# Performance work log

Hardware: AMD Instinct MI355X
Metric: run time of the kernel (lower is better)

Reference implementation:

```python
import jax, jax.numpy as jnp
import numpy as np

N_FOOD = 50000
N_NUT = 50000
E = 800000
D = 128      # embedding_dim == hidden_dim
H = 4        # heads
C = D // H   # per-head channels
L = 2        # num_layers
NEG_SLOPE = 0.2


def _gat_conv(x_src, x_dst, ei, Wsrc, Wdst, a_src, a_dst, bias, n_dst):
    """PyG GATConv (bipartite, no self loops, concat heads, no edge_dim)."""
    hs = (x_src @ Wsrc).reshape(-1, H, C)   # [Ns, H, C]
    hd = (x_dst @ Wdst).reshape(-1, H, C)   # [Nd, H, C]
    src, dst = ei[0], ei[1]
    alpha_s = jnp.einsum('nhc,hc->nh', hs, a_src)  # [Ns, H]
    alpha_d = jnp.einsum('nhc,hc->nh', hd, a_dst)  # [Nd, H]
    e = alpha_s[src] + alpha_d[dst]                # [E, H]
    e = jax.nn.leaky_relu(e, NEG_SLOPE)
    # segment softmax over edges grouped by destination node
    emax = jax.ops.segment_max(e, dst, num_segments=n_dst)
    emax = jnp.where(jnp.isfinite(emax), emax, 0.0)
    ex = jnp.exp(e - emax[dst])
    denom = jax.ops.segment_sum(ex, dst, num_segments=n_dst)
    alpha = ex / (denom[dst] + 1e-16)              # [E, H]
    msg = hs[src] * alpha[:, :, None]              # [E, H, C]
    out = jax.ops.segment_sum(msg, dst, num_segments=n_dst)
    return out.reshape(n_dst, H * C) + bias


def setup_inputs() -> dict:
    key = jax.random.key(0)
    ks = jax.random.split(key, 16)
    w = 1.0 / np.sqrt(D)
    a = 1.0 / np.sqrt(C)
    inp = {
        'x_food': jax.random.normal(ks[0], (N_FOOD, D), jnp.float32),
        'x_nut': jax.random.normal(ks[1], (N_NUT, D), jnp.float32),
        'Wsrc_fn': jax.random.normal(ks[2], (L, D, D), jnp.float32) * w,
        'Wdst_fn': jax.random.normal(ks[3], (L, D, D), jnp.float32) * w,
        'att_src_fn': jax.random.normal(ks[4], (L, H, C), jnp.float32) * a,
        'att_dst_fn': jax.random.normal(ks[5], (L, H, C), jnp.float32) * a,
        'bias_fn': jnp.zeros((L, D), jnp.float32),
        'Wsrc_nf': jax.random.normal(ks[6], (L, D, D), jnp.float32) * w,
        'Wdst_nf': jax.random.normal(ks[7], (L, D, D), jnp.float32) * w,
        'att_src_nf': jax.random.normal(ks[8], (L, H, C), jnp.float32) * a,
        'att_dst_nf': jax.random.normal(ks[9], (L, H, C), jnp.float32) * a,
        'bias_nf': jnp.zeros((L, D), jnp.float32),
        'ei_fn': jax.random.randint(ks[10], (2, E), 0, N_FOOD, jnp.int32),  # food -> nutrient
        'ei_nf': jax.random.randint(ks[11], (2, E), 0, N_NUT, jnp.int32),   # nutrient -> food
    }
    return inp


def reference(x_food, x_nut, Wsrc_fn, Wdst_fn, att_src_fn, att_dst_fn, bias_fn,
              Wsrc_nf, Wdst_nf, att_src_nf, att_dst_nf, bias_nf, ei_fn, ei_nf):
    h_food, h_nut = x_food, x_nut
    for l in range(L):
        # relation food --contains--> nutrient (dst = nutrient)
        out_nut = _gat_conv(h_food, h_nut, ei_fn, Wsrc_fn[l], Wdst_fn[l],
                            att_src_fn[l], att_dst_fn[l], bias_fn[l], N_NUT)
        # relation nutrient --contained_in--> food (dst = food)
        out_food = _gat_conv(h_nut, h_food, ei_nf, Wsrc_nf[l], Wdst_nf[l],
                             att_src_nf[l], att_dst_nf[l], bias_nf[l], N_FOOD)
        # dropout is identity at inference; ELU activation
        h_food = jax.nn.elu(out_food)
        h_nut = jax.nn.elu(out_nut)
    return jnp.stack([h_food, h_nut])  # [2, 50000, 128]
```

## Files before the change

### kernel.cpp

```cpp
#include <hip/hip_runtime.h>
#include <math.h>

#define NNODE 50000
#define NEDGE 800000
#define DIM   128
#define NHEAD 4
#define NTILE ((NNODE + 63) / 64)
#define NBUCK 196
#define ECHUNK 196
#define CAP   6144
#define LOG2E 1.44269504088896340736f

typedef __bf16 bf16x8 __attribute__((ext_vector_type(8)));
typedef float  f32x4  __attribute__((ext_vector_type(4)));
typedef float  f32x2  __attribute__((ext_vector_type(2)));

static __device__ __forceinline__ void bfsplit(float x, ushort& hi, ushort& lo) {
    __bf16 h = (__bf16)x;
    float hf = (float)h;
    __bf16 l = (__bf16)(x - hf);
    hi = __builtin_bit_cast(unsigned short, h);
    lo = __builtin_bit_cast(unsigned short, l);
}
static __device__ __forceinline__ ushort f2h(float x) {
    _Float16 h = (_Float16)x;
    return __builtin_bit_cast(unsigned short, h);
}
static __device__ __forceinline__ f32x2 up2v(unsigned u) {
    f32x2 r;
    r.x = (float)__builtin_bit_cast(_Float16, (unsigned short)(u & 0xffff));
    r.y = (float)__builtin_bit_cast(_Float16, (unsigned short)(u >> 16));
    return r;
}
static __device__ __forceinline__ unsigned encf(float f) {
    unsigned u = __builtin_bit_cast(unsigned, f);
    return (u >> 31) ? ~u : (u | 0x80000000u);
}
static __device__ __forceinline__ float decf(unsigned x) {
    unsigned u = (x >> 31) ? (x & 0x7fffffffu) : ~x;
    return __builtin_bit_cast(float, u);
}

__global__ __launch_bounds__(256) void bhist(const int* __restrict__ eA,
                                             const int* __restrict__ eB,
                                             int* __restrict__ bcnt) {
    int rel = (int)(blockIdx.x >= ECHUNK);
    const int* dstrow = (rel ? eB : eA) + NEDGE;
    int blk = blockIdx.x - rel * ECHUNK;
    __shared__ int hist[256];
    hist[threadIdx.x] = 0;
    __syncthreads();
    int base = blk * 4096;
    #pragma unroll
    for (int k = 0; k < 16; k++) {
        int e = base + k * 256 + threadIdx.x;
        if (e < NEDGE) atomicAdd(&hist[dstrow[e] >> 8], 1);
    }
    __syncthreads();
    int h = hist[threadIdx.x];
    if (h) atomicAdd(&bcnt[rel * 256 + threadIdx.x], h);
}

__global__ __launch_bounds__(256) void bscan(const int* __restrict__ bcnt,
                                             int* __restrict__ bko, int* __restrict__ bcur,
                                             int* __restrict__ ptrA, int* __restrict__ ptrB) {
    int rel = blockIdx.x;
    __shared__ int tmp[256];
    int t = threadIdx.x;
    int v = bcnt[rel * 256 + t];
    tmp[t] = v; __syncthreads();
    for (int off = 1; off < 256; off <<= 1) {
        int a = (t >= off) ? tmp[t - off] : 0; __syncthreads();
        tmp[t] += a; __syncthreads();
    }
    int excl = tmp[t] - v;
    bko[rel * 256 + t] = excl;
    bcur[rel * 256 + t] = excl;
    if (t == 255) (rel ? ptrB : ptrA)[NNODE] = tmp[255];
}

__global__ __launch_bounds__(256) void bscatter(const int* __restrict__ eA,
                                                const int* __restrict__ eB,
                                                int* __restrict__ bcur,
                                                unsigned* __restrict__ bktA,
                                                unsigned* __restrict__ bktB) {
    int rel = (int)(blockIdx.x >= ECHUNK);
    const int* ebase = rel ? eB : eA;
    unsigned* bkt = rel ? bktB : bktA;
    int blk = blockIdx.x - rel * ECHUNK;
    __shared__ int hist[256], bas[256], cur[256];
    hist[threadIdx.x] = 0;
    __syncthreads();
    int base = blk * 4096;
    #pragma unroll
    for (int k = 0; k < 16; k++) {
        int e = base + k * 256 + threadIdx.x;
        if (e < NEDGE) atomicAdd(&hist[ebase[NEDGE + e] >> 8], 1);
    }
    __syncthreads();
    int h = hist[threadIdx.x];
    bas[threadIdx.x] = h ? atomicAdd(&bcur[rel * 256 + threadIdx.x], h) : 0;
    cur[threadIdx.x] = 0;
    __syncthreads();
    #pragma unroll
    for (int k = 0; k < 16; k++) {
        int e = base + k * 256 + threadIdx.x;
        if (e < NEDGE) {
            int s = ebase[e], d = ebase[NEDGE + e];
            int b = d >> 8;
            int loc = atomicAdd(&cur[b], 1);
            bkt[bas[b] + loc] = ((unsigned)(d & 255) << 16) | (unsigned)s;
        }
    }
}

__global__ __launch_bounds__(256) void bsort(const unsigned* __restrict__ bktA,
                                             const unsigned* __restrict__ bktB,
                                             const int* __restrict__ bko,
                                             int* __restrict__ ptrA, int* __restrict__ ptrB,
                                             ushort* __restrict__ srcA, ushort* __restrict__ srcB) {
    int rel = (int)(blockIdx.x >= NBUCK);
    const unsigned* bkt = rel ? bktB : bktA;
    int* ptr   = rel ? ptrB : ptrA;
    ushort* srcs = rel ? srcB : srcA;
    int b = blockIdx.x - rel * NBUCK;
    int beg = bko[rel * 256 + b], end = bko[rel * 256 + b + 1];
    int cnt_e = end - beg;
    __shared__ int hist[256], excl[256], cur[256];
    __shared__ unsigned sorted[CAP];
    int t = threadIdx.x;
    hist[t] = 0;
    __syncthreads();
    for (int i = t; i < cnt_e; i += 256) atomicAdd(&hist[bkt[beg + i] >> 16], 1);
    __syncthreads();
    int v = hist[t];
    excl[t] = v; __syncthreads();
    for (int off = 1; off < 256; off <<= 1) {
        int a = (t >= off) ? excl[t - off] : 0; __syncthreads();
        excl[t] += a; __syncthreads();
    }
    int ex = excl[t] - v;
    int d = b * 256 + t;
    if (d < NNODE) ptr[d] = beg + ex;
    cur[t] = ex;
    __syncthreads();
    for (int i = t; i < cnt_e; i += 256) {
        unsigned u = bkt[beg + i];
        int dl = u >> 16;
        int p = atomicAdd(&cur[dl], 1);
        if (p < CAP) sorted[p] = u;
        else srcs[beg + p] = (ushort)(u & 0xffffu);
    }
    __syncthreads();
    int lim = cnt_e < CAP ? cnt_e : CAP;
    for (int i = t; i < lim; i += 256) {
        unsigned u = sorted[i];
        srcs[beg + i] = (ushort)(u & 0xffffu);
    }
}

__global__ void prep_wav(const float* __restrict__ Wsrc_fn, const float* __restrict__ a_src_fn,
                         const float* __restrict__ Wdst_fn, const float* __restrict__ a_dst_fn,
                         const float* __restrict__ Wsrc_nf, const float* __restrict__ a_src_nf,
                         const float* __restrict__ Wdst_nf, const float* __restrict__ a_dst_nf,
                         float* __restrict__ wav) {
    int call = blockIdx.x;
    int layer = call >> 1, which = call & 1;
    const float* Ws = which ? Wsrc_nf : Wsrc_fn;
    const float* as = which ? a_src_nf : a_src_fn;
    const float* Wd = which ? Wdst_fn : Wdst_nf;
    const float* ad = which ? a_dst_fn : a_dst_nf;
    Ws += layer * DIM * DIM; Wd += layer * DIM * DIM;
    as += layer * DIM; ad += layer * DIM;
    for (int it = threadIdx.x; it < 512; it += 256) {
        int k = it >> 2, h = it & 3;
        float s = 0.f, dv = 0.f;
        #pragma unroll 8
        for (int c = 0; c < 32; c++) {
            s  += Ws[k * DIM + h * 32 + c] * as[h * 32 + c];
            dv += Wd[k * DIM + h * 32 + c] * ad[h * 32 + c];
        }
        float* o = wav + (size_t)call * DIM * 8 + k * 8;
        o[h] = s; o[h + 4] = dv;
    }
}

__global__ __launch_bounds__(256, 3) void transform_kernel(
    const float* __restrict__ XA, const float* __restrict__ WA, const float* __restrict__ wavA,
    ushort* __restrict__ HSA, float* __restrict__ ASA, float* __restrict__ ADA,
    const float* __restrict__ XB, const float* __restrict__ WB, const float* __restrict__ wavB,
    ushort* __restrict__ HSB, float* __restrict__ ASB, float* __restrict__ ADB,
    unsigned* __restrict__ Mg, int nb)
{
    int rel = (int)(blockIdx.x >= (unsigned)nb);
    const float* X  = rel ? XB : XA;
    const float* W  = rel ? WB : WA;
    const float* wav = rel ? wavB : wavA;
    ushort* HS = rel ? HSB : HSA;
    float*  AS = rel ? ASB : ASA;
    float*  AD = rel ? ADB : ADA;

    __shared__ ushort WTh[64][136], WTl[64][136];
    __shared__ ushort wavTh[16][136], wavTl[16][136];
    __shared__ unsigned mloc[4];

    int vb = blockIdx.x - rel * nb;
    int half = vb & 1;
    int ch = half * 64;

    for (int i = threadIdx.x; i < 64 * DIM; i += 256) {
        int col = i & 63, k = i >> 6;
        ushort hi, lo; bfsplit(W[k * DIM + ch + col], hi, lo);
        WTh[col][k] = hi; WTl[col][k] = lo;
    }
    for (int i = threadIdx.x; i < 16 * DIM; i += 256) {
        int c = i & 15, k = i >> 4;
        float w = (c < 8) ? wav[k * 8 + c] : 0.f;
        ushort hi, lo; bfsplit(w, hi, lo);
        wavTh[c][k] = hi; wavTl[c][k] = lo;
    }
    if (threadIdx.x < 4) mloc[threadIdx.x] = 0;
    __syncthreads();

    const int wv = threadIdx.x >> 6, lane = threadIdx.x & 63;
    const int lm = lane & 15, lq = lane >> 4;
    const int r0 = wv * 16;

    for (int tile = vb >> 1; tile < NTILE; tile += (nb >> 1)) {
        int row0 = tile * 64;
        int myrow = row0 + r0 + lm;
        int rowc = myrow < NNODE ? myrow : NNODE - 1;
        const float4* Xr = (const float4*)(X + (size_t)rowc * DIM);

        float4 xv[8];
        #pragma unroll
        for (int kc = 0; kc < 4; kc++) {
            xv[kc * 2]     = Xr[kc * 8 + lq * 2];
            xv[kc * 2 + 1] = Xr[kc * 8 + lq * 2 + 1];
        }

        f32x4 acc[4] = {{0,0,0,0},{0,0,0,0},{0,0,0,0},{0,0,0,0}};
        f32x4 accv = {0,0,0,0};
        #pragma unroll
        for (int kc = 0; kc < 4; kc++) {
            const float* fp = (const float*)&xv[kc * 2];
            bf16x8 ah, al;
            #pragma unroll
            for (int j = 0; j < 8; j++) {
                float x = fp[j];
                __bf16 h = (__bf16)x;
                ah[j] = h;
                al[j] = (__bf16)(x - (float)h);
            }
            int k0 = kc * 32 + lq * 8;
            #pragma unroll
            for (int ct = 0; ct < 4; ct++) {
                bf16x8 bh = *(const bf16x8*)&WTh[ct * 16 + lm][k0];
                bf16x8 bl = *(const bf16x8*)&WTl[ct * 16 + lm][k0];
                acc[ct] = __builtin_amdgcn_mfma_f32_16x16x32_bf16(al, bh, acc[ct], 0, 0, 0);
                acc[ct] = __builtin_amdgcn_mfma_f32_16x16x32_bf16(ah, bl, acc[ct], 0, 0, 0);
                acc[ct] = __builtin_amdgcn_mfma_f32_16x16x32_bf16(ah, bh, acc[ct], 0, 0, 0);
            }
            if (half == 0) {
                bf16x8 vh = *(const bf16x8*)&wavTh[lm][k0];
                bf16x8 vl = *(const bf16x8*)&wavTl[lm][k0];
                accv = __builtin_amdgcn_mfma_f32_16x16x32_bf16(al, vh, accv, 0, 0, 0);
                accv = __builtin_amdgcn_mfma_f32_16x16x32_bf16(ah, vl, accv, 0, 0, 0);
                accv = __builtin_amdgcn_mfma_f32_16x16x32_bf16(ah, vh, accv, 0, 0, 0);
            }
        }

        #pragma unroll
        for (int ct = 0; ct < 4; ct++) {
            #pragma unroll
            for (int r = 0; r < 4; r++) {
                int row = row0 + r0 + lq * 4 + r;
                if (row < NNODE) HS[(size_t)row * DIM + ch + ct * 16 + lm] = f2h(acc[ct][r]);
            }
        }
        if (half == 0 && lm < 8) {
            accv *= LOG2E;
            float mx4 = -INFINITY;
            #pragma unroll
            for (int r = 0; r < 4; r++) {
                int row = row0 + r0 + lq * 4 + r;
                if (row < NNODE) {
                    if (lm < 4) AS[row * 4 + lm] = accv[r];
                    else        AD[row * 4 + (lm - 4)] = accv[r];
                }
                mx4 = fmaxf(mx4, accv[r]);
            }
            if (lm < 4) atomicMax(&mloc[lm], encf(mx4));
        }
    }
    __syncthreads();
    if (half == 0 && threadIdx.x < 4)
        atomicMax(&Mg[rel * 4 + threadIdx.x], mloc[threadIdx.x]);
}

__global__ __launch_bounds__(256) void agg_kernel(
    const ushort* __restrict__ HSA, const float* __restrict__ ASA, const float* __restrict__ ADA,
    const int* __restrict__ ptrA, const ushort* __restrict__ srcA,
    const float* __restrict__ biasA, float* __restrict__ outA,
    const ushort* __restrict__ HSB, const float* __restrict__ ASB, const float* __restrict__ ADB,
    const int* __restrict__ ptrB, const ushort* __restrict__ srcB,
    const float* __restrict__ biasB, float* __restrict__ outB,
    const unsigned* __restrict__ Mg, int nb)
{
    int rel = (int)(blockIdx.x >= (unsigned)nb);
    const uint4* HS4 = (const uint4*)(rel ? HSB : HSA);
    const float* AS = rel ? ASB : ASA;
    const float* AD = rel ? ADB : ADA;
    const ushort* srcs = rel ? srcB : srcA;
    const int* ptr = rel ? ptrB : ptrA;
    const float* bias = rel ? biasB : biasA;
    float* out = rel ? outB : outA;

    int bid = blockIdx.x - rel * nb;
    int wave = threadIdx.x >> 6, lane = threadIdx.x & 63;
    int d = bid * 4 + wave;
    if (d >= NNODE) return;

    int q  = lane >> 4;
    int li = lane & 15;
    int hh = li >> 2;

    float ad_h = AD[d * 4 + hh];
    float mm = decf(Mg[rel * 4 + hh]) + ad_h;
    mm = mm > 0.f ? mm : 0.2f * mm;

    int e0 = ptr[d], e1 = ptr[d + 1];

    float acc[8] = {0.f,0.f,0.f,0.f,0.f,0.f,0.f,0.f};
    float l = 0.f;

    int e = e0;
    for (; e + 8 <= e1; e += 8) {
        int iA = e + q, iB = e + 4 + q;
        int sA = srcs[iA], sB = srcs[iB];
        uint4 hA = HS4[sA * 16 + li];
        uint4 hB = HS4[sB * 16 + li];
        float aA = AS[sA * 4 + hh];
        float aB = AS[sB * 4 + hh];
        float vA = aA + ad_h; vA = fmaxf(vA, 0.2f * vA);
        float vB = aB + ad_h; vB = fmaxf(vB, 0.2f * vB);
        float pA = __builtin_amdgcn_exp2f(vA - mm);
        float pB = __builtin_amdgcn_exp2f(vB - mm);
        l += pA + pB;
        #pragma unroll
        for (int j = 0; j < 4; j++) {
            f32x2 h2A = up2v(((const unsigned*)&hA)[j]);
            f32x2 h2B = up2v(((const unsigned*)&hB)[j]);
            acc[2*j]   += h2A.x * pA + h2B.x * pB;
            acc[2*j+1] += h2A.y * pA + h2B.y * pB;
        }
    }
    for (; e < e1; e += 4) {
        int ee = e + q;
        bool act = ee < e1;
        int eidx = act ? ee : e1 - 1;
        int s = srcs[eidx];
        uint4 hv = HS4[s * 16 + li];
        float av = AS[s * 4 + hh];
        float v = av + ad_h; v = fmaxf(v, 0.2f * v);
        float p = __builtin_amdgcn_exp2f(v - mm);
        p = act ? p : 0.f;
        l += p;
        #pragma unroll
        for (int j = 0; j < 4; j++) {
            f32x2 h2 = up2v(((const unsigned*)&hv)[j]);
            acc[2*j]   += h2.x * p;
            acc[2*j+1] += h2.y * p;
        }
    }

    #pragma unroll
    for (int j = 0; j < 8; j++) {
        acc[j] += __shfl_xor(acc[j], 16, 64);
        acc[j] += __shfl_xor(acc[j], 32, 64);
    }
    l += __shfl_xor(l, 16, 64);
    l += __shfl_xor(l, 32, 64);

    if (q == 0) {
        float inv = 1.f / (l + 1e-16f);
        const float4* b4 = (const float4*)bias + li * 2;
        float4 b0 = b4[0], b1 = b4[1];
        float o[8];
        o[0] = acc[0] * inv + b0.x; o[1] = acc[1] * inv + b0.y;
        o[2] = acc[2] * inv + b0.z; o[3] = acc[3] * inv + b0.w;
        o[4] = acc[4] * inv + b1.x; o[5] = acc[5] * inv + b1.y;
        o[6] = acc[6] * inv + b1.z; o[7] = acc[7] * inv + b1.w;
        #pragma unroll
        for (int j = 0; j < 8; j++)
            o[j] = o[j] > 0.f ? o[j] : __expf(o[j]) - 1.f;
        float4* o4 = (float4*)(out + (size_t)d * DIM) + li * 2;
        o4[0] = make_float4(o[0], o[1], o[2], o[3]);
        o4[1] = make_float4(o[4], o[5], o[6], o[7]);
    }
}

extern "C" void kernel_launch(void* const* d_in, const int* in_sizes, int n_in,
                              void* d_out, int out_size, void* d_ws, size_t ws_size,
                              hipStream_t stream) {
    const float* x_food      = (const float*)d_in[0];
    const float* x_nut       = (const float*)d_in[1];
    const float* Wsrc_fn     = (const float*)d_in[2];
    const float* Wdst_fn     = (const float*)d_in[3];
    const float* att_src_fn  = (const float*)d_in[4];
    const float* att_dst_fn  = (const float*)d_in[5];
    const float* bias_fn     = (const float*)d_in[6];
    const float* Wsrc_nf     = (const float*)d_in[7];
    const float* Wdst_nf     = (const float*)d_in[8];
    const float* att_src_nf  = (const float*)d_in[9];
    const float* att_dst_nf  = (const float*)d_in[10];
    const float* bias_nf     = (const float*)d_in[11];
    const int*   ei_fn       = (const int*)d_in[12];
    const int*   ei_nf       = (const int*)d_in[13];
    float* out = (float*)d_out;

    char* ws = (char*)d_ws;
    size_t off = 0;
    auto alloc_f = [&](size_t n) { float* p = (float*)(ws + off); off += n * 4; return p; };
    auto alloc_i = [&](size_t n) { int* p = (int*)(ws + off); off += n * 4; return p; };
    auto alloc_u = [&](size_t n) { ushort* p = (ushort*)(ws + off); off += n * 2; return p; };

    float* B_food = alloc_f((size_t)NNODE * DIM);
    float* B_nut  = alloc_f((size_t)NNODE * DIM);
    ushort* HS_fn = alloc_u((size_t)NNODE * DIM);
    ushort* HS_nf = alloc_u((size_t)NNODE * DIM);
    float* AS_fn  = alloc_f(NNODE * NHEAD);
    float* AS_nf  = alloc_f(NNODE * NHEAD);
    float* AD_fn  = alloc_f(NNODE * NHEAD);
    float* AD_nf  = alloc_f(NNODE * NHEAD);
    float* wav    = alloc_f(4 * DIM * 8);
    int* ptr_fn   = alloc_i(50004);
    int* ptr_nf   = alloc_i(50004);
    ushort* srcs_fn = alloc_u(NEDGE);
    ushort* srcs_nf = alloc_u(NEDGE);
    int* bcnt     = alloc_i(512);
    unsigned* Mbuf = (unsigned*)alloc_i(16);
    int* bko      = alloc_i(512);
    int* bcur     = alloc_i(512);
    unsigned* bkt_fn = (unsigned*)B_food;
    unsigned* bkt_nf = (unsigned*)B_nut;

    hipMemsetAsync(bcnt, 0, (512 + 16) * 4, stream);
    bhist<<<2 * ECHUNK, 256, 0, stream>>>(ei_fn, ei_nf, bcnt);
    bscan<<<2, 256, 0, stream>>>(bcnt, bko, bcur, ptr_fn, ptr_nf);
    bscatter<<<2 * ECHUNK, 256, 0, stream>>>(ei_fn, ei_nf, bcur, bkt_fn, bkt_nf);
    bsort<<<2 * NBUCK, 256, 0, stream>>>(bkt_fn, bkt_nf, bko, ptr_fn, ptr_nf,
                                         srcs_fn, srcs_nf);

    prep_wav<<<4, 256, 0, stream>>>(Wsrc_fn, att_src_fn, Wdst_fn, att_dst_fn,
                                    Wsrc_nf, att_src_nf, Wdst_nf, att_dst_nf, wav);

    const int WL = DIM * DIM;
    const int TNB = 768;
    const int ANB = (NNODE + 3) / 4;
    float* wav0 = wav;
    float* wav1 = wav + DIM * 8;
    float* wav2 = wav + 2 * DIM * 8;
    float* wav3 = wav + 3 * DIM * 8;

    transform_kernel<<<2 * TNB, 256, 0, stream>>>(
        x_food, Wsrc_fn, wav0, HS_fn, AS_fn, AD_nf,
        x_nut,  Wsrc_nf, wav1, HS_nf, AS_nf, AD_fn, Mbuf, TNB);
    agg_kernel<<<2 * ANB, 256, 0, stream>>>(
        HS_fn, AS_fn, AD_fn, ptr_fn, srcs_fn, bias_fn, B_nut,
        HS_nf, AS_nf, AD_nf, ptr_nf, srcs_nf, bias_nf, B_food, Mbuf, ANB);

    transform_kernel<<<2 * TNB, 256, 0, stream>>>(
        B_food, Wsrc_fn + WL, wav2, HS_fn, AS_fn, AD_nf,
        B_nut,  Wsrc_nf + WL, wav3, HS_nf, AS_nf, AD_fn, Mbuf + 8, TNB);
    agg_kernel<<<2 * ANB, 256, 0, stream>>>(
        HS_fn, AS_fn, AD_fn, ptr_fn, srcs_fn, bias_fn + DIM, out + (size_t)NNODE * DIM,
        HS_nf, AS_nf, AD_nf, ptr_nf, srcs_nf, bias_nf + DIM, out, Mbuf + 8, ANB);
}
```

Before: 423.5 us.

## Double-buffer X loads, stage HS stores through LDS, halve transform grid

The transform kernel now prefetches the next tile's X rows into registers while the current tile is computed, which is meant to hide global-load latency. Output HS values are staged through a shared-memory tile so each thread writes a coalesced 16-byte vector instead of scattered 2-byte stores. The wav split is skipped for the half that does not use it, and the block count per relation drops from 768 to 384 so each block loops over more tiles. The cost is two extra block barriers per tile, more registers for the second X buffer, extra LDS, and fewer resident blocks.

New measurement: 356.7 us. 1.19x faster.

```diff
diff --git a/kernel.cpp b/kernel.cpp
--- a/kernel.cpp
+++ b/kernel.cpp
@@ -202,6 +202,7 @@
 
     __shared__ ushort WTh[64][136], WTl[64][136];
     __shared__ ushort wavTh[16][136], wavTl[16][136];
+    __shared__ ushort hsb[64][72];
     __shared__ unsigned mloc[4];
 
     int vb = blockIdx.x - rel * nb;
@@ -213,11 +214,13 @@
         ushort hi, lo; bfsplit(W[k * DIM + ch + col], hi, lo);
         WTh[col][k] = hi; WTl[col][k] = lo;
     }
-    for (int i = threadIdx.x; i < 16 * DIM; i += 256) {
-        int c = i & 15, k = i >> 4;
-        float w = (c < 8) ? wav[k * 8 + c] : 0.f;
-        ushort hi, lo; bfsplit(w, hi, lo);
-        wavTh[c][k] = hi; wavTl[c][k] = lo;
+    if (half == 0) {
+        for (int i = threadIdx.x; i < 16 * DIM; i += 256) {
+            int c = i & 15, k = i >> 4;
+            float w = (c < 8) ? wav[k * 8 + c] : 0.f;
+            ushort hi, lo; bfsplit(w, hi, lo);
+            wavTh[c][k] = hi; wavTl[c][k] = lo;
+        }
     }
     if (threadIdx.x < 4) mloc[threadIdx.x] = 0;
     __syncthreads();
@@ -225,20 +228,21 @@
     const int wv = threadIdx.x >> 6, lane = threadIdx.x & 63;
     const int lm = lane & 15, lq = lane >> 4;
     const int r0 = wv * 16;
-
-    for (int tile = vb >> 1; tile < NTILE; tile += (nb >> 1)) {
-        int row0 = tile * 64;
-        int myrow = row0 + r0 + lm;
+    const int tstride = nb >> 1;
+
+    auto loadX = [&](int tile, float4* dst) {
+        int myrow = tile * 64 + r0 + lm;
         int rowc = myrow < NNODE ? myrow : NNODE - 1;
         const float4* Xr = (const float4*)(X + (size_t)rowc * DIM);
-
-        float4 xv[8];
         #pragma unroll
         for (int kc = 0; kc < 4; kc++) {
-            xv[kc * 2]     = Xr[kc * 8 + lq * 2];
-            xv[kc * 2 + 1] = Xr[kc * 8 + lq * 2 + 1];
-        }
-
+            dst[kc * 2]     = Xr[kc * 8 + lq * 2];
+            dst[kc * 2 + 1] = Xr[kc * 8 + lq * 2 + 1];
+        }
+    };
+
+    auto computeTile = [&](const float4* xv, int tile) {
+        int row0 = tile * 64;
         f32x4 acc[4] = {{0,0,0,0},{0,0,0,0},{0,0,0,0},{0,0,0,0}};
         f32x4 accv = {0,0,0,0};
         #pragma unroll
@@ -270,14 +274,6 @@
             }
         }
 
-        #pragma unroll
-        for (int ct = 0; ct < 4; ct++) {
-            #pragma unroll
-            for (int r = 0; r < 4; r++) {
-                int row = row0 + r0 + lq * 4 + r;
-                if (row < NNODE) HS[(size_t)row * DIM + ch + ct * 16 + lm] = f2h(acc[ct][r]);
-            }
-        }
         if (half == 0 && lm < 8) {
             accv *= LOG2E;
             float mx4 = -INFINITY;
@@ -292,7 +288,38 @@
             }
             if (lm < 4) atomicMax(&mloc[lm], encf(mx4));
         }
-    }
+
+        __syncthreads();
+        #pragma unroll
+        for (int ct = 0; ct < 4; ct++) {
+            #pragma unroll
+            for (int r = 0; r < 4; r++)
+                hsb[r0 + lq * 4 + r][ct * 16 + lm] = f2h(acc[ct][r]);
+        }
+        __syncthreads();
+        #pragma unroll
+        for (int p = 0; p < 2; p++) {
+            int idx = p * 256 + (int)threadIdx.x;
+            int lr = idx >> 3, off = (idx & 7) * 8;
+            int rg = row0 + lr;
+            if (rg < NNODE)
+                *(uint4*)(HS + (size_t)rg * DIM + ch + off) = *(const uint4*)&hsb[lr][off];
+        }
+    };
+
+    float4 xa[8], xb[8];
+    int tile = vb >> 1;
+    loadX(tile, xa);
+    while (tile < NTILE) {
+        if (tile + tstride < NTILE) loadX(tile + tstride, xb);
+        computeTile(xa, tile);
+        tile += tstride;
+        if (tile >= NTILE) break;
+        if (tile + tstride < NTILE) loadX(tile + tstride, xa);
+        computeTile(xb, tile);
+        tile += tstride;
+    }
+
     __syncthreads();
     if (half == 0 && threadIdx.x < 4)
         atomicMax(&Mg[rel * 4 + threadIdx.x], mloc[threadIdx.x]);
@@ -456,7 +483,7 @@
                                     Wsrc_nf, att_src_nf, Wdst_nf, att_dst_nf, wav);
 
     const int WL = DIM * DIM;
-    const int TNB = 768;
+    const int TNB = 384;
     const int ANB = (NNODE + 3) / 4;
     float* wav0 = wav;
     float* wav1 = wav + DIM * 8;
```
